# Optimization experiments

Measured on AMD Instinct MI355X. Metric: run time of the kernel, lower is better.

Reference implementation:

```python
import jax, jax.numpy as jnp
import numpy as np

B, N, IN_CH = 16, 2048, 128
H, C = 4, 64
HC = H * C
E = 524288
NT = B * N
FC0, FC1 = 1024, 512
OMIC = 128
OUT = 2
LN_EPS = 1e-5


def setup_inputs() -> dict:
    key = jax.random.key(0)
    ks = jax.random.split(key, 32)
    s = 0.02
    d = {}
    d['x'] = jax.random.normal(ks[0], (NT, IN_CH), jnp.float32)
    d['edge_index'] = jax.random.randint(ks[1], (2, E), 0, NT, dtype=jnp.int64)
    # GATConv 1: Linear(IN_CH, H*C, bias=False), att_src/att_dst [H,C], bias [H*C]
    d['w1'] = jax.random.normal(ks[2], (IN_CH, HC), jnp.float32) * s
    d['att_src1'] = jax.random.normal(ks[3], (H, C), jnp.float32) * s
    d['att_dst1'] = jax.random.normal(ks[4], (H, C), jnp.float32) * s
    d['bias1'] = jnp.zeros((HC,), jnp.float32)
    d['pool1_w'] = jax.random.normal(ks[5], (HC, 1), jnp.float32) * s
    d['pool1_b'] = jnp.zeros((1,), jnp.float32)
    # GATConv 2: in = H*C
    d['w2'] = jax.random.normal(ks[6], (HC, HC), jnp.float32) * s
    d['att_src2'] = jax.random.normal(ks[7], (H, C), jnp.float32) * s
    d['att_dst2'] = jax.random.normal(ks[8], (H, C), jnp.float32) * s
    d['bias2'] = jnp.zeros((HC,), jnp.float32)
    d['pool2_w'] = jax.random.normal(ks[9], (HC, 1), jnp.float32) * s
    d['pool2_b'] = jnp.zeros((1,), jnp.float32)
    # LayerNorm(num_nodes)
    d['ln_w'] = jnp.ones((N,), jnp.float32)
    d['ln_b'] = jnp.zeros((N,), jnp.float32)
    # FC encoder: Linear(3N, FC0)+ELU, Linear(FC0, FC1)+ELU, Linear(FC1, OMIC)+ELU
    d['enc0_w'] = jax.random.normal(ks[10], (3 * N, FC0), jnp.float32) * s
    d['enc0_b'] = jnp.zeros((FC0,), jnp.float32)
    d['enc1_w'] = jax.random.normal(ks[11], (FC0, FC1), jnp.float32) * s
    d['enc1_b'] = jnp.zeros((FC1,), jnp.float32)
    d['enc2_w'] = jax.random.normal(ks[12], (FC1, OMIC), jnp.float32) * s
    d['enc2_b'] = jnp.zeros((OMIC,), jnp.float32)
    d['last_w'] = jax.random.normal(ks[13], (OMIC, OUT), jnp.float32) * s
    d['last_b'] = jnp.zeros((OUT,), jnp.float32)
    return d


def layer_norm(v, w, b):
    mu = jnp.mean(v, axis=-1, keepdims=True)
    var = jnp.mean((v - mu) ** 2, axis=-1, keepdims=True)
    return (v - mu) * jax.lax.rsqrt(var + LN_EPS) * w + b


def gat_conv(x, src, dst, w, att_src, att_dst, bias):
    # x: [NT, F_in] -> transformed per head [NT, H, C]
    xw = (x @ w).reshape(NT, H, C)
    a_src = jnp.einsum('nhc,hc->nh', xw, att_src)  # [NT, H]
    a_dst = jnp.einsum('nhc,hc->nh', xw, att_dst)
    alpha = jax.nn.leaky_relu(a_src[src] + a_dst[dst], negative_slope=0.2)  # [E', H]
    amax = jax.ops.segment_max(alpha, dst, num_segments=NT)
    ea = jnp.exp(alpha - amax[dst])
    denom = jax.ops.segment_sum(ea, dst, num_segments=NT)
    coef = ea / (denom[dst] + 1e-16)
    msg = xw[src] * coef[:, :, None]  # [E', H, C]
    out = jax.ops.segment_sum(msg, dst, num_segments=NT)
    return out.reshape(NT, HC) + bias


def reference(x, edge_index, w1, att_src1, att_dst1, bias1, pool1_w, pool1_b,
              w2, att_src2, att_dst2, bias2, pool2_w, pool2_b,
              ln_w, ln_b, enc0_w, enc0_b, enc1_w, enc1_b, enc2_w, enc2_b,
              last_w, last_b):
    # add self-loops (GATConv default)
    loops = jnp.arange(NT, dtype=edge_index.dtype)
    src = jnp.concatenate([edge_index[0], loops])
    dst = jnp.concatenate([edge_index[1], loops])
    # layer1 feature: per-node mean, densified to [B, N]
    x0 = layer_norm(jnp.mean(x, axis=-1).reshape(B, N), ln_w, ln_b)
    # GAT layer 1 (dropout is identity in eval)
    h = jax.nn.elu(gat_conv(x, src, dst, w1, att_src1, att_dst1, bias1))
    x1 = layer_norm((h @ pool1_w + pool1_b)[:, 0].reshape(B, N), ln_w, ln_b)
    # GAT layer 2
    h = jax.nn.elu(gat_conv(h, src, dst, w2, att_src2, att_dst2, bias2))
    x2 = layer_norm((h @ pool2_w + pool2_b)[:, 0].reshape(B, N), ln_w, ln_b)
    feat = jnp.concatenate([x0, x1, x2], axis=1)  # [B, 3N]
    e = jax.nn.elu(feat @ enc0_w + enc0_b)
    e = jax.nn.elu(e @ enc1_w + enc1_b)
    e = jax.nn.elu(e @ enc2_w + enc2_b)
    return e @ last_w + last_b  # [B, OUT]
```

## Files before the change

### kernel.cpp

```cpp
#include <hip/hip_runtime.h>
#include <math.h>

#define NTN 32768
#define BB 16
#define NN 2048
#define IN_CH 128
#define HC 256
#define EREAL 524288
#define ETOT (EREAL + NTN)
#define FC0 1024
#define FC1 512
#define OMIC 128
#define OUTD 2
#define CAP 96

#define PREP_BLKS (NTN / 4)
#define DEG_BLKS (EREAL / 256)
#define CASTW_BLKS ((HC * IN_CH + HC * HC) / 256)
#define GEMM_YB (NTN / 128)
#define FILL_YB 512

typedef __attribute__((ext_vector_type(8))) short bf16x8;
typedef __attribute__((ext_vector_type(4))) float f32x4;
typedef __attribute__((ext_vector_type(2))) float f32x2;

static __device__ __forceinline__ float wave_sum(float v) {
    for (int o = 32; o; o >>= 1) v += __shfl_xor(v, o);
    return v;
}
static __device__ __forceinline__ unsigned short f2bf(float f) {
    unsigned u = __float_as_uint(f);
    unsigned r = (u + 0x7fff + ((u >> 16) & 1)) >> 16;
    return (unsigned short)r;
}
static __device__ __forceinline__ void pkfma(f32x2& acc, f32x2 ab, f32x2 e2) {
    asm("v_pk_fma_f32 %0, %1, %2, %0" : "+v"(acc) : "v"(ab), "v"(e2));
}
static __device__ __forceinline__ void fma8pk(uint4 v, f32x2 e2, f32x2* acc) {
    f32x2 p;
    p.x = __uint_as_float(v.x << 16); p.y = __uint_as_float(v.x & 0xffff0000u);
    pkfma(acc[0], p, e2);
    p.x = __uint_as_float(v.y << 16); p.y = __uint_as_float(v.y & 0xffff0000u);
    pkfma(acc[1], p, e2);
    p.x = __uint_as_float(v.z << 16); p.y = __uint_as_float(v.z & 0xffff0000u);
    pkfma(acc[2], p, e2);
    p.x = __uint_as_float(v.w << 16); p.y = __uint_as_float(v.w & 0xffff0000u);
    pkfma(acc[3], p, e2);
}
static __device__ __forceinline__ void dot2bf(float& acc, unsigned px, unsigned pe) {
    asm("v_dot2_f32_bf16 %0, %1, %2, %0" : "+v"(acc) : "v"(px), "v"(pe));
}
static __device__ __forceinline__ void dot8x2(uint4 a, uint4 b, unsigned pe, float* acc) {
    unsigned p;
    p = __builtin_amdgcn_perm(a.x, b.x, 0x01000504u); dot2bf(acc[0], p, pe);
    p = __builtin_amdgcn_perm(a.x, b.x, 0x03020706u); dot2bf(acc[1], p, pe);
    p = __builtin_amdgcn_perm(a.y, b.y, 0x01000504u); dot2bf(acc[2], p, pe);
    p = __builtin_amdgcn_perm(a.y, b.y, 0x03020706u); dot2bf(acc[3], p, pe);
    p = __builtin_amdgcn_perm(a.z, b.z, 0x01000504u); dot2bf(acc[4], p, pe);
    p = __builtin_amdgcn_perm(a.z, b.z, 0x03020706u); dot2bf(acc[5], p, pe);
    p = __builtin_amdgcn_perm(a.w, b.w, 0x01000504u); dot2bf(acc[6], p, pe);
    p = __builtin_amdgcn_perm(a.w, b.w, 0x03020706u); dot2bf(acc[7], p, pe);
}

__global__ __launch_bounds__(256) void k_pre(
    const float* __restrict__ x, unsigned short* __restrict__ xb, float* __restrict__ xmean,
    const int* __restrict__ ei, int* __restrict__ deg, int* __restrict__ epos,
    const float* __restrict__ w1, const float* __restrict__ w2,
    unsigned short* __restrict__ w1t, unsigned short* __restrict__ w2t) {
    int b = blockIdx.x, t = threadIdx.x;
    if (b < PREP_BLKS) {
        int wave = t >> 6, lane = t & 63;
        int n = b * 4 + wave;
        float2 v = *(const float2*)(x + (size_t)n * IN_CH + lane * 2);
        ushort2 o;
        o.x = f2bf(v.x); o.y = f2bf(v.y);
        *(ushort2*)(xb + (size_t)n * IN_CH + lane * 2) = o;
        float s = wave_sum(v.x + v.y);
        if (lane == 0) xmean[n] = s * (1.0f / 128.0f);
    } else if (b < PREP_BLKS + DEG_BLKS) {
        int e = (b - PREP_BLKS) * 256 + t;
        int d = ei[EREAL + e];
        epos[e] = atomicAdd(&deg[d], 1);
    } else {
        int idx = (b - PREP_BLKS - DEG_BLKS) * 256 + t;
        if (idx < HC * IN_CH) {
            int n = idx / IN_CH, k = idx % IN_CH;
            w1t[idx] = f2bf(w1[(size_t)k * HC + n]);
        } else {
            int j = idx - HC * IN_CH;
            int n = j / HC, k = j % HC;
            w2t[j] = f2bf(w2[(size_t)k * HC + n]);
        }
    }
}

__global__ __launch_bounds__(1024) void k_scan(const int* __restrict__ deg, int* __restrict__ rowptr,
                                               int* __restrict__ csr) {
    __shared__ int sd[1024];
    int t = threadIdx.x;
    int base = t * 32;
    int loc[32];
    int s = 0;
#pragma unroll
    for (int j = 0; j < 32; j++) { int d = deg[base + j] + 1; loc[j] = d; s += d; }
    sd[t] = s; __syncthreads();
    for (int o = 1; o < 1024; o <<= 1) {
        int v = (t >= o) ? sd[t - o] : 0;
        __syncthreads();
        sd[t] += v;
        __syncthreads();
    }
    int run = sd[t] - s;
#pragma unroll
    for (int j = 0; j < 32; j++) {
        rowptr[base + j] = run;
        csr[run] = base + j;
        run += loc[j];
    }
    if (t == 1023) rowptr[NTN] = run;
}

__global__ __launch_bounds__(256) void k_gemm_mfma(
    const unsigned short* __restrict__ A, const unsigned short* __restrict__ Bt, int K,
    const float* __restrict__ attS, const float* __restrict__ attD,
    unsigned short* __restrict__ Cout, float* __restrict__ aS, float* __restrict__ aD,
    const int* __restrict__ ei, const int* __restrict__ epos,
    const int* __restrict__ rowptr, int* __restrict__ csr) {
    __shared__ unsigned short As[128][72];
    __shared__ unsigned short Bs[64][72];
    const int t = threadIdx.x;
    const int bx = blockIdx.x, by = blockIdx.y;
    if (by >= GEMM_YB) {
        int e = (((by - GEMM_YB) * 4 + bx)) * 256 + t;
        int s = ei[e], d = ei[EREAL + e];
        csr[rowptr[d] + 1 + epos[e]] = s;
        return;
    }
    const int lane = t & 63, wave = t >> 6;
    const int quad = lane >> 4, l16 = lane & 15;
    const int arow = t >> 1, acol = (t & 1) * 32;
    const int brow = t >> 2, bcol = (t & 3) * 16;
    const unsigned short* Ag = A + (size_t)(by * 128 + arow) * K + acol;
    const unsigned short* Bg = Bt + (size_t)(bx * 64 + brow) * K + bcol;
    f32x4 acc[2][4] = {};
    for (int k0 = 0; k0 < K; k0 += 64) {
        uint4 a0 = *(const uint4*)(Ag + k0);
        uint4 a1 = *(const uint4*)(Ag + k0 + 8);
        uint4 a2 = *(const uint4*)(Ag + k0 + 16);
        uint4 a3 = *(const uint4*)(Ag + k0 + 24);
        uint4 b0 = *(const uint4*)(Bg + k0);
        uint4 b1 = *(const uint4*)(Bg + k0 + 8);
        __syncthreads();
        *(uint4*)&As[arow][acol +  0] = a0;
        *(uint4*)&As[arow][acol +  8] = a1;
        *(uint4*)&As[arow][acol + 16] = a2;
        *(uint4*)&As[arow][acol + 24] = a3;
        *(uint4*)&Bs[brow][bcol +  0] = b0;
        *(uint4*)&Bs[brow][bcol +  8] = b1;
        __syncthreads();
#pragma unroll
        for (int kc = 0; kc < 64; kc += 32) {
            bf16x8 af[2], bfr[4];
#pragma unroll
            for (int mt = 0; mt < 2; mt++)
                af[mt] = *(const bf16x8*)&As[wave * 32 + mt * 16 + l16][kc + quad * 8];
#pragma unroll
            for (int nt = 0; nt < 4; nt++)
                bfr[nt] = *(const bf16x8*)&Bs[nt * 16 + l16][kc + quad * 8];
#pragma unroll
            for (int mt = 0; mt < 2; mt++)
#pragma unroll
                for (int nt = 0; nt < 4; nt++)
                    acc[mt][nt] = __builtin_amdgcn_mfma_f32_16x16x32_bf16(af[mt], bfr[nt], acc[mt][nt], 0, 0, 0);
        }
    }
    float as_l[4], ad_l[4];
#pragma unroll
    for (int nt = 0; nt < 4; nt++) {
        int gcol = bx * 64 + nt * 16 + l16;
        as_l[nt] = attS[gcol];
        ad_l[nt] = attD[gcol];
    }
#pragma unroll
    for (int mt = 0; mt < 2; mt++) {
#pragma unroll
        for (int reg = 0; reg < 4; reg++) {
            int grow = by * 128 + wave * 32 + mt * 16 + quad * 4 + reg;
            float ps = 0.f, pd = 0.f;
#pragma unroll
            for (int nt = 0; nt < 4; nt++) {
                float v = acc[mt][nt][reg];
                Cout[(size_t)grow * HC + bx * 64 + nt * 16 + l16] = f2bf(v);
                ps += v * as_l[nt];
                pd += v * ad_l[nt];
            }
            for (int o = 8; o; o >>= 1) { ps += __shfl_xor(ps, o); pd += __shfl_xor(pd, o); }
            if (l16 == 0) { aS[grow * 4 + bx] = ps; aD[grow * 4 + bx] = pd; }
        }
    }
}

__global__ __launch_bounds__(256) void k_agg(
    const unsigned short* __restrict__ xw, const float* __restrict__ aS, const float* __restrict__ aD,
    const int* __restrict__ rowptr, const int* __restrict__ csr,
    const float* __restrict__ bias, const float* __restrict__ poolw, const float* __restrict__ poolb,
    unsigned short* __restrict__ hout, float* __restrict__ xpre) {
    __shared__ float ea_s[2][CAP][4];
    __shared__ float part[2][2][256];
    __shared__ float lpart[2][2][4];
    int t = threadIdx.x;
    int wave = t >> 6, lane = t & 63;
    int nd = wave >> 1, half = wave & 1;
    int n = blockIdx.x * 2 + nd;
    int beg = rowptr[n], end = rowptr[n + 1];
    int deg = end - beg;
    int mid = beg + ((deg + 1) >> 1);
    int wbeg = half ? mid : beg;
    int wend = half ? end : mid;
    float4 ad4 = *(const float4*)(aD + n * 4);
    if (deg <= CAP) {
        for (int i = wbeg + lane; i < wend; i += 64) {
            int s = csr[i];
            float4 as4 = *(const float4*)(aS + s * 4);
            float a0 = as4.x + ad4.x; a0 = a0 > 0.f ? a0 : 0.2f * a0;
            float a1 = as4.y + ad4.y; a1 = a1 > 0.f ? a1 : 0.2f * a1;
            float a2 = as4.z + ad4.z; a2 = a2 > 0.f ? a2 : 0.2f * a2;
            float a3 = as4.w + ad4.w; a3 = a3 > 0.f ? a3 : 0.2f * a3;
            float4 e4;
            e4.x = __expf(a0); e4.y = __expf(a1); e4.z = __expf(a2); e4.w = __expf(a3);
            *(float4*)&ea_s[nd][i - beg][0] = e4;
        }
    } else {
        float l0 = 0.f, l1 = 0.f, l2 = 0.f, l3 = 0.f;
        for (int i = wbeg + lane; i < wend; i += 64) {
            int s = csr[i];
            float4 as4 = *(const float4*)(aS + s * 4);
            float a0 = as4.x + ad4.x; a0 = a0 > 0.f ? a0 : 0.2f * a0; l0 += __expf(a0);
            float a1 = as4.y + ad4.y; a1 = a1 > 0.f ? a1 : 0.2f * a1; l1 += __expf(a1);
            float a2 = as4.z + ad4.z; a2 = a2 > 0.f ? a2 : 0.2f * a2; l2 += __expf(a2);
            float a3 = as4.w + ad4.w; a3 = a3 > 0.f ? a3 : 0.2f * a3; l3 += __expf(a3);
        }
        l0 = wave_sum(l0); l1 = wave_sum(l1); l2 = wave_sum(l2); l3 = wave_sum(l3);
        if (lane == 0) {
            lpart[nd][half][0] = l0; lpart[nd][half][1] = l1;
            lpart[nd][half][2] = l2; lpart[nd][half][3] = l3;
        }
    }
    __syncthreads();
    int l31 = lane & 31, hi = lane >> 5;
    int head = l31 >> 3;
    float acc8[8] = {};
    f32x2 accF[4] = {};
    unsigned t8 = (unsigned)(l31 * 8);
    if (deg <= CAP) {
        int i = wbeg;
        for (; i + 4 <= wend; i += 4) {
            int iA = i + 2 * hi;
            int sA = csr[iA], sB = csr[iA + 1];
            float eA = ea_s[nd][iA - beg][head];
            float eB = ea_s[nd][iA + 1 - beg][head];
            unsigned pe;
            asm("v_cvt_pk_bf16_f32 %0, %1, %2" : "=v"(pe) : "v"(eA), "v"(eB));
            uint4 vA = *(const uint4*)(xw + ((unsigned)sA * HC + t8));
            uint4 vB = *(const uint4*)(xw + ((unsigned)sB * HC + t8));
            dot8x2(vA, vB, pe, acc8);
        }
        if (i < wend) {
            int iA = i + 2 * hi, iB = iA + 1;
            bool okA = iA < wend, okB = iB < wend;
            int ia = iA - beg; if (ia > CAP - 1) ia = CAP - 1;
            int ib = iB - beg; if (ib > CAP - 1) ib = CAP - 1;
            int sA = csr[okA ? iA : wbeg];
            int sB = csr[okB ? iB : wbeg];
            float eA = okA ? ea_s[nd][ia][head] : 0.f;
            float eB = okB ? ea_s[nd][ib][head] : 0.f;
            unsigned pe;
            asm("v_cvt_pk_bf16_f32 %0, %1, %2" : "=v"(pe) : "v"(eA), "v"(eB));
            uint4 vA = *(const uint4*)(xw + ((unsigned)sA * HC + t8));
            uint4 vB = *(const uint4*)(xw + ((unsigned)sB * HC + t8));
            dot8x2(vA, vB, pe, acc8);
        }
    } else {
        const unsigned short* xwc = xw + t8;
        float adh = head == 0 ? ad4.x : head == 1 ? ad4.y : head == 2 ? ad4.z : ad4.w;
        for (int i = wbeg; i < wend; i += 2) {
            int idx = i + hi;
            bool ok = idx < wend;
            int sA = csr[ok ? idx : wbeg];
            float a = aS[sA * 4 + head] + adh;
            a = a > 0.f ? a : 0.2f * a;
            float eA = ok ? __expf(a) : 0.f;
            uint4 vA = *(const uint4*)(xwc + (size_t)sA * HC);
            f32x2 eA2; eA2.x = eA; eA2.y = eA;
            fma8pk(vA, eA2, accF);
        }
    }
    float r8[8];
#pragma unroll
    for (int j = 0; j < 8; j++) {
        float v = acc8[j] + accF[j >> 1][j & 1];
        v += __shfl_xor(v, 32);
        r8[j] = v;
    }
    if (hi == 0) {
        float4 q0; q0.x = r8[0]; q0.y = r8[1]; q0.z = r8[2]; q0.w = r8[3];
        float4 q1; q1.x = r8[4]; q1.y = r8[5]; q1.z = r8[6]; q1.w = r8[7];
        *(float4*)&part[nd][half][l31 * 8] = q0;
        *(float4*)&part[nd][half][l31 * 8 + 4] = q1;
    }
    __syncthreads();
    if (half == 0 && hi == 0) {
        float ilh;
        if (deg <= CAP) {
            float lsum = 0.f;
            for (int j = (l31 & 7); j < deg; j += 8) lsum += ea_s[nd][j][head];
            lsum += __shfl_xor(lsum, 1);
            lsum += __shfl_xor(lsum, 2);
            lsum += __shfl_xor(lsum, 4);
            ilh = 1.0f / (lsum + 1e-16f);
        } else {
            ilh = 1.0f / (lpart[nd][0][head] + lpart[nd][1][head] + 1e-16f);
        }
        float4 p00 = *(const float4*)&part[nd][0][l31 * 8];
        float4 p01 = *(const float4*)&part[nd][0][l31 * 8 + 4];
        float4 p10 = *(const float4*)&part[nd][1][l31 * 8];
        float4 p11 = *(const float4*)&part[nd][1][l31 * 8 + 4];
        float4 b0 = *(const float4*)(bias + l31 * 8);
        float4 b1 = *(const float4*)(bias + l31 * 8 + 4);
        float r[8];
        r[0] = (p00.x + p10.x) * ilh + b0.x;
        r[1] = (p00.y + p10.y) * ilh + b0.y;
        r[2] = (p00.z + p10.z) * ilh + b0.z;
        r[3] = (p00.w + p10.w) * ilh + b0.w;
        r[4] = (p01.x + p11.x) * ilh + b1.x;
        r[5] = (p01.y + p11.y) * ilh + b1.y;
        r[6] = (p01.z + p11.z) * ilh + b1.z;
        r[7] = (p01.w + p11.w) * ilh + b1.w;
#pragma unroll
        for (int j = 0; j < 8; j++) r[j] = r[j] > 0.f ? r[j] : expm1f(r[j]);
        if (hout) {
            uint4 o;
            o.x = (unsigned)f2bf(r[0]) | ((unsigned)f2bf(r[1]) << 16);
            o.y = (unsigned)f2bf(r[2]) | ((unsigned)f2bf(r[3]) << 16);
            o.z = (unsigned)f2bf(r[4]) | ((unsigned)f2bf(r[5]) << 16);
            o.w = (unsigned)f2bf(r[6]) | ((unsigned)f2bf(r[7]) << 16);
            *(uint4*)(hout + (size_t)n * HC + l31 * 8) = o;
        }
        float4 w0 = *(const float4*)(poolw + l31 * 8);
        float4 w1v = *(const float4*)(poolw + l31 * 8 + 4);
        float p = r[0] * w0.x + r[1] * w0.y + r[2] * w0.z + r[3] * w0.w +
                  r[4] * w1v.x + r[5] * w1v.y + r[6] * w1v.z + r[7] * w1v.w;
        for (int o = 16; o; o >>= 1) p += __shfl_xor(p, o);
        if (l31 == 0) xpre[n] = p + poolb[0];
    }
}

__global__ __launch_bounds__(256) void k_ln3(const float* __restrict__ xmean, const float* __restrict__ x1pre,
                                             const float* __restrict__ x2pre, const float* __restrict__ lw,
                                             const float* __restrict__ lb, float* __restrict__ feat) {
    __shared__ float r0[256], r1[256];
    int b = blockIdx.x, t = threadIdx.x;
    int row = b & 15, seg = b >> 4;
    const float* src = (seg == 0 ? xmean : seg == 1 ? x1pre : x2pre) + (size_t)row * NN;
    float* dst = feat + (size_t)row * (3 * NN) + seg * NN;
    float v[8];
    float s = 0.f, s2 = 0.f;
#pragma unroll
    for (int j = 0; j < 8; j++) {
        float x = src[t + j * 256];
        v[j] = x; s += x; s2 += x * x;
    }
    r0[t] = s; r1[t] = s2; __syncthreads();
    for (int o = 128; o; o >>= 1) {
        if (t < o) { r0[t] += r0[t + o]; r1[t] += r1[t + o]; }
        __syncthreads();
    }
    float mu = r0[0] * (1.0f / NN);
    float var = r1[0] * (1.0f / NN) - mu * mu;
    float rs = rsqrtf(var + 1e-5f);
#pragma unroll
    for (int j = 0; j < 8; j++) {
        int idx = t + j * 256;
        dst[idx] = (v[j] - mu) * rs * lw[idx] + lb[idx];
    }
}

template<int KC>
__global__ __launch_bounds__(256) void k_fc_splitk(const float* __restrict__ In, const float* __restrict__ W,
                                                   float* __restrict__ partial, int K, int Nc) {
    __shared__ float in_s[16][KC];
    int t = threadIdx.x;
    int k0 = blockIdx.y * KC;
    for (int idx = t; idx < 16 * KC; idx += 256) {
        int r = idx / KC, kk = idx % KC;
        in_s[r][kk] = In[(size_t)r * K + k0 + kk];
    }
    __syncthreads();
    int col = blockIdx.x * 256 + t;
    if (col < Nc) {
        float acc[16] = {};
#pragma unroll
        for (int kk = 0; kk < KC; kk++) {
            float w = W[(size_t)(k0 + kk) * Nc + col];
#pragma unroll
            for (int r = 0; r < 16; r++) acc[r] += in_s[r][kk] * w;
        }
        float* pp = partial + ((size_t)blockIdx.y * 16) * Nc + col;
#pragma unroll
        for (int r = 0; r < 16; r++) pp[(size_t)r * Nc] = acc[r];
    }
}

template<int KS>
__global__ __launch_bounds__(256) void k_fc_reduce(const float* __restrict__ partial, const float* __restrict__ bias,
                                                   float* __restrict__ Out, int Nc) {
    __shared__ float sm[256];
    int t = threadIdx.x;
    int col = blockIdx.x * 32 + (t & 31);
    int r = blockIdx.y;
    int h = t >> 5;
    float s = 0.f;
#pragma unroll
    for (int i = 0; i < KS / 8; i++)
        s += partial[((size_t)(h + 8 * i) * 16 + r) * Nc + col];
    sm[t] = s;
    __syncthreads();
    if (t < 32) {
        float v = sm[t] + sm[t + 32] + sm[t + 64] + sm[t + 96] +
                  sm[t + 128] + sm[t + 160] + sm[t + 192] + sm[t + 224];
        v += bias[col];
        v = v > 0.f ? v : expm1f(v);
        Out[(size_t)r * Nc + col] = v;
    }
}

__global__ __launch_bounds__(256) void k_last(const float* __restrict__ In, const float* __restrict__ W,
                                              const float* __restrict__ b, float* __restrict__ Out) {
    int t = threadIdx.x;
    int r = t >> 4, c = (t >> 3) & 1, ksub = t & 7;
    float s = 0.f;
#pragma unroll
    for (int k = 0; k < OMIC / 8; k++) s += In[r * OMIC + k * 8 + ksub] * W[(k * 8 + ksub) * OUTD + c];
    for (int o = 1; o < 8; o <<= 1) s += __shfl_xor(s, o);
    if (ksub == 0) Out[r * OUTD + c] = s + b[c];
}

extern "C" void kernel_launch(void* const* d_in, const int* in_sizes, int n_in,
                              void* d_out, int out_size, void* d_ws, size_t ws_size,
                              hipStream_t stream) {
    (void)in_sizes; (void)n_in; (void)out_size; (void)ws_size;
    const float* x        = (const float*)d_in[0];
    const int*   ei       = (const int*)d_in[1];
    const float* w1       = (const float*)d_in[2];
    const float* att_src1 = (const float*)d_in[3];
    const float* att_dst1 = (const float*)d_in[4];
    const float* bias1    = (const float*)d_in[5];
    const float* pool1_w  = (const float*)d_in[6];
    const float* pool1_b  = (const float*)d_in[7];
    const float* w2       = (const float*)d_in[8];
    const float* att_src2 = (const float*)d_in[9];
    const float* att_dst2 = (const float*)d_in[10];
    const float* bias2    = (const float*)d_in[11];
    const float* pool2_w  = (const float*)d_in[12];
    const float* pool2_b  = (const float*)d_in[13];
    const float* ln_w     = (const float*)d_in[14];
    const float* ln_b     = (const float*)d_in[15];
    const float* enc0_w   = (const float*)d_in[16];
    const float* enc0_b   = (const float*)d_in[17];
    const float* enc1_w   = (const float*)d_in[18];
    const float* enc1_b   = (const float*)d_in[19];
    const float* enc2_w   = (const float*)d_in[20];
    const float* enc2_b   = (const float*)d_in[21];
    const float* last_w   = (const float*)d_in[22];
    const float* last_b   = (const float*)d_in[23];
    float* out = (float*)d_out;

    char* p = (char*)d_ws;
    auto alloc = [&](size_t bytes) -> void* {
        void* r = (void*)p;
        p += (bytes + 255) & ~(size_t)255;
        return r;
    };
    unsigned short* xwb  = (unsigned short*)alloc((size_t)NTN * HC * 2);
    unsigned short* hb   = (unsigned short*)alloc((size_t)NTN * HC * 2);
    unsigned short* xb   = (unsigned short*)alloc((size_t)NTN * IN_CH * 2);
    unsigned short* w1t  = (unsigned short*)alloc((size_t)HC * IN_CH * 2);
    unsigned short* w2t  = (unsigned short*)alloc((size_t)HC * HC * 2);
    float* a_src  = (float*)alloc((size_t)NTN * 4 * 4);
    float* a_dst  = (float*)alloc((size_t)NTN * 4 * 4);
    float* xmean  = (float*)alloc((size_t)NTN * 4);
    float* x1pre  = (float*)alloc((size_t)NTN * 4);
    float* x2pre  = (float*)alloc((size_t)NTN * 4);
    float* feat   = (float*)alloc((size_t)BB * 3 * NN * 4);
    float* e0     = (float*)alloc((size_t)BB * FC0 * 4);
    float* e1     = (float*)alloc((size_t)BB * FC1 * 4);
    float* e2     = (float*)alloc((size_t)BB * OMIC * 4);
    float* part0  = (float*)alloc((size_t)96 * 16 * FC0 * 4);
    float* part1  = (float*)alloc((size_t)64 * 16 * FC1 * 4);
    float* part2  = (float*)alloc((size_t)32 * 16 * OMIC * 4);
    int*   deg    = (int*)alloc((size_t)NTN * 4);
    int*   rowptr = (int*)alloc((size_t)(NTN + 1) * 4);
    int*   epos   = (int*)alloc((size_t)EREAL * 4);
    int*   csr    = (int*)alloc((size_t)ETOT * 4);

    hipMemsetAsync(deg, 0, (size_t)NTN * 4, stream);

    k_pre<<<PREP_BLKS + DEG_BLKS + CASTW_BLKS, 256, 0, stream>>>(
        x, xb, xmean, ei, deg, epos, w1, w2, w1t, w2t);
    k_scan<<<1, 1024, 0, stream>>>(deg, rowptr, csr);

    k_gemm_mfma<<<dim3(4, GEMM_YB + FILL_YB), 256, 0, stream>>>(
        xb, w1t, IN_CH, att_src1, att_dst1, xwb, a_src, a_dst, ei, epos, rowptr, csr);
    k_agg<<<NTN / 2, 256, 0, stream>>>(xwb, a_src, a_dst, rowptr, csr, bias1, pool1_w, pool1_b, hb, x1pre);

    k_gemm_mfma<<<dim3(4, GEMM_YB), 256, 0, stream>>>(
        hb, w2t, HC, att_src2, att_dst2, xwb, a_src, a_dst, ei, epos, rowptr, csr);
    k_agg<<<NTN / 2, 256, 0, stream>>>(xwb, a_src, a_dst, rowptr, csr, bias2, pool2_w, pool2_b, (unsigned short*)nullptr, x2pre);

    k_ln3<<<48, 256, 0, stream>>>(xmean, x1pre, x2pre, ln_w, ln_b, feat);

    k_fc_splitk<64><<<dim3(4, 96), 256, 0, stream>>>(feat, enc0_w, part0, 3 * NN, FC0);
    k_fc_reduce<96><<<dim3(FC0 / 32, 16), 256, 0, stream>>>(part0, enc0_b, e0, FC0);
    k_fc_splitk<16><<<dim3(2, 64), 256, 0, stream>>>(e0, enc1_w, part1, FC0, FC1);
    k_fc_reduce<64><<<dim3(FC1 / 32, 16), 256, 0, stream>>>(part1, enc1_b, e1, FC1);
    k_fc_splitk<16><<<dim3(1, 32), 256, 0, stream>>>(e1, enc2_w, part2, FC1, OMIC);
    k_fc_reduce<32><<<dim3(OMIC / 32, 16), 256, 0, stream>>>(part2, enc2_b, e2, OMIC);
    k_last<<<1, 256, 0, stream>>>(e2, last_w, last_b, out);
}
```

Before: 340.6 us.

## Assign one wave per node in GAT aggregation and deepen gather unrolling

The aggregation kernel now handles four nodes per block, one wavefront per node, instead of splitting each node's edges across two waves. This removes the cross-wave LDS partial-sum exchange and both block-wide barriers. Source byte offsets are cached in LDS so the gather loop no longer rereads csr, and the main loop is unrolled to gather 16 neighbor rows per iteration to keep more loads in flight. In exchange, each node's edge loop runs serially within a single wave, and the extra unrolling raises register pressure.

Result: faster. 315.7 us (-7.3%).

```diff
diff --git a/kernel.cpp b/kernel.cpp
--- a/kernel.cpp
+++ b/kernel.cpp
@@ -32,6 +32,10 @@
     unsigned u = __float_as_uint(f);
     unsigned r = (u + 0x7fff + ((u >> 16) & 1)) >> 16;
     return (unsigned short)r;
+}
+static __device__ __forceinline__ void wave_sync() {
+    asm volatile("s_waitcnt lgkmcnt(0)" ::: "memory");
+    __builtin_amdgcn_sched_barrier(0);
 }
 static __device__ __forceinline__ void pkfma(f32x2& acc, f32x2 ab, f32x2 e2) {
     asm("v_pk_fma_f32 %0, %1, %2, %0" : "+v"(acc) : "v"(ab), "v"(e2));
@@ -205,22 +209,19 @@
     const int* __restrict__ rowptr, const int* __restrict__ csr,
     const float* __restrict__ bias, const float* __restrict__ poolw, const float* __restrict__ poolb,
     unsigned short* __restrict__ hout, float* __restrict__ xpre) {
-    __shared__ float ea_s[2][CAP][4];
-    __shared__ float part[2][2][256];
-    __shared__ float lpart[2][2][4];
+    __shared__ float ea_s[4][CAP][4];
+    __shared__ int   ss[4][CAP];
     int t = threadIdx.x;
-    int wave = t >> 6, lane = t & 63;
-    int nd = wave >> 1, half = wave & 1;
-    int n = blockIdx.x * 2 + nd;
+    int w = t >> 6, lane = t & 63;
+    int n = blockIdx.x * 4 + w;
     int beg = rowptr[n], end = rowptr[n + 1];
     int deg = end - beg;
-    int mid = beg + ((deg + 1) >> 1);
-    int wbeg = half ? mid : beg;
-    int wend = half ? end : mid;
     float4 ad4 = *(const float4*)(aD + n * 4);
+    float l0 = 0.f, l1 = 0.f, l2 = 0.f, l3 = 0.f;
     if (deg <= CAP) {
-        for (int i = wbeg + lane; i < wend; i += 64) {
-            int s = csr[i];
+        for (int i = lane; i < deg; i += 64) {
+            int s = csr[beg + i];
+            ss[w][i] = s << 9;
             float4 as4 = *(const float4*)(aS + s * 4);
             float a0 = as4.x + ad4.x; a0 = a0 > 0.f ? a0 : 0.2f * a0;
             float a1 = as4.y + ad4.y; a1 = a1 > 0.f ? a1 : 0.2f * a1;
@@ -228,12 +229,12 @@
             float a3 = as4.w + ad4.w; a3 = a3 > 0.f ? a3 : 0.2f * a3;
             float4 e4;
             e4.x = __expf(a0); e4.y = __expf(a1); e4.z = __expf(a2); e4.w = __expf(a3);
-            *(float4*)&ea_s[nd][i - beg][0] = e4;
-        }
+            *(float4*)&ea_s[w][i][0] = e4;
+        }
+        wave_sync();
     } else {
-        float l0 = 0.f, l1 = 0.f, l2 = 0.f, l3 = 0.f;
-        for (int i = wbeg + lane; i < wend; i += 64) {
-            int s = csr[i];
+        for (int i = lane; i < deg; i += 64) {
+            int s = csr[beg + i];
             float4 as4 = *(const float4*)(aS + s * 4);
             float a0 = as4.x + ad4.x; a0 = a0 > 0.f ? a0 : 0.2f * a0; l0 += __expf(a0);
             float a1 = as4.y + ad4.y; a1 = a1 > 0.f ? a1 : 0.2f * a1; l1 += __expf(a1);
@@ -241,52 +242,87 @@
             float a3 = as4.w + ad4.w; a3 = a3 > 0.f ? a3 : 0.2f * a3; l3 += __expf(a3);
         }
         l0 = wave_sum(l0); l1 = wave_sum(l1); l2 = wave_sum(l2); l3 = wave_sum(l3);
-        if (lane == 0) {
-            lpart[nd][half][0] = l0; lpart[nd][half][1] = l1;
-            lpart[nd][half][2] = l2; lpart[nd][half][3] = l3;
-        }
-    }
-    __syncthreads();
+    }
     int l31 = lane & 31, hi = lane >> 5;
     int head = l31 >> 3;
     float acc8[8] = {};
     f32x2 accF[4] = {};
-    unsigned t8 = (unsigned)(l31 * 8);
+    unsigned tb = (unsigned)(l31 * 16);
+    const char* xwb_ = (const char*)xw;
     if (deg <= CAP) {
-        int i = wbeg;
-        for (; i + 4 <= wend; i += 4) {
+        int i = 0;
+        for (; i + 16 <= deg; i += 16) {
+            int iA = i + 8 * hi;
+            int o0 = ss[w][iA], o1 = ss[w][iA + 1], o2 = ss[w][iA + 2], o3 = ss[w][iA + 3];
+            int o4 = ss[w][iA + 4], o5 = ss[w][iA + 5], o6 = ss[w][iA + 6], o7 = ss[w][iA + 7];
+            float e0 = ea_s[w][iA][head],     e1 = ea_s[w][iA + 1][head];
+            float e2 = ea_s[w][iA + 2][head], e3 = ea_s[w][iA + 3][head];
+            float e4 = ea_s[w][iA + 4][head], e5 = ea_s[w][iA + 5][head];
+            float e6 = ea_s[w][iA + 6][head], e7 = ea_s[w][iA + 7][head];
+            uint4 v0 = *(const uint4*)(xwb_ + ((unsigned)o0 + tb));
+            uint4 v1 = *(const uint4*)(xwb_ + ((unsigned)o1 + tb));
+            uint4 v2 = *(const uint4*)(xwb_ + ((unsigned)o2 + tb));
+            uint4 v3 = *(const uint4*)(xwb_ + ((unsigned)o3 + tb));
+            uint4 v4 = *(const uint4*)(xwb_ + ((unsigned)o4 + tb));
+            uint4 v5 = *(const uint4*)(xwb_ + ((unsigned)o5 + tb));
+            uint4 v6 = *(const uint4*)(xwb_ + ((unsigned)o6 + tb));
+            uint4 v7 = *(const uint4*)(xwb_ + ((unsigned)o7 + tb));
+            unsigned p01, p23, p45, p67;
+            asm("v_cvt_pk_bf16_f32 %0, %1, %2" : "=v"(p01) : "v"(e0), "v"(e1));
+            asm("v_cvt_pk_bf16_f32 %0, %1, %2" : "=v"(p23) : "v"(e2), "v"(e3));
+            asm("v_cvt_pk_bf16_f32 %0, %1, %2" : "=v"(p45) : "v"(e4), "v"(e5));
+            asm("v_cvt_pk_bf16_f32 %0, %1, %2" : "=v"(p67) : "v"(e6), "v"(e7));
+            dot8x2(v0, v1, p01, acc8);
+            dot8x2(v2, v3, p23, acc8);
+            dot8x2(v4, v5, p45, acc8);
+            dot8x2(v6, v7, p67, acc8);
+        }
+        for (; i + 8 <= deg; i += 8) {
+            int iA = i + 4 * hi;
+            int o0 = ss[w][iA], o1 = ss[w][iA + 1], o2 = ss[w][iA + 2], o3 = ss[w][iA + 3];
+            float e0 = ea_s[w][iA][head],     e1 = ea_s[w][iA + 1][head];
+            float e2 = ea_s[w][iA + 2][head], e3 = ea_s[w][iA + 3][head];
+            uint4 v0 = *(const uint4*)(xwb_ + ((unsigned)o0 + tb));
+            uint4 v1 = *(const uint4*)(xwb_ + ((unsigned)o1 + tb));
+            uint4 v2 = *(const uint4*)(xwb_ + ((unsigned)o2 + tb));
+            uint4 v3 = *(const uint4*)(xwb_ + ((unsigned)o3 + tb));
+            unsigned p01, p23;
+            asm("v_cvt_pk_bf16_f32 %0, %1, %2" : "=v"(p01) : "v"(e0), "v"(e1));
+            asm("v_cvt_pk_bf16_f32 %0, %1, %2" : "=v"(p23) : "v"(e2), "v"(e3));
+            dot8x2(v0, v1, p01, acc8);
+            dot8x2(v2, v3, p23, acc8);
+        }
+        for (; i + 4 <= deg; i += 4) {
             int iA = i + 2 * hi;
-            int sA = csr[iA], sB = csr[iA + 1];
-            float eA = ea_s[nd][iA - beg][head];
-            float eB = ea_s[nd][iA + 1 - beg][head];
+            int o0 = ss[w][iA], o1 = ss[w][iA + 1];
+            float e0 = ea_s[w][iA][head], e1 = ea_s[w][iA + 1][head];
             unsigned pe;
-            asm("v_cvt_pk_bf16_f32 %0, %1, %2" : "=v"(pe) : "v"(eA), "v"(eB));
-            uint4 vA = *(const uint4*)(xw + ((unsigned)sA * HC + t8));
-            uint4 vB = *(const uint4*)(xw + ((unsigned)sB * HC + t8));
-            dot8x2(vA, vB, pe, acc8);
-        }
-        if (i < wend) {
+            asm("v_cvt_pk_bf16_f32 %0, %1, %2" : "=v"(pe) : "v"(e0), "v"(e1));
+            uint4 v0 = *(const uint4*)(xwb_ + ((unsigned)o0 + tb));
+            uint4 v1 = *(const uint4*)(xwb_ + ((unsigned)o1 + tb));
+            dot8x2(v0, v1, pe, acc8);
+        }
+        if (i < deg) {
             int iA = i + 2 * hi, iB = iA + 1;
-            bool okA = iA < wend, okB = iB < wend;
-            int ia = iA - beg; if (ia > CAP - 1) ia = CAP - 1;
-            int ib = iB - beg; if (ib > CAP - 1) ib = CAP - 1;
-            int sA = csr[okA ? iA : wbeg];
-            int sB = csr[okB ? iB : wbeg];
-            float eA = okA ? ea_s[nd][ia][head] : 0.f;
-            float eB = okB ? ea_s[nd][ib][head] : 0.f;
+            bool okA = iA < deg, okB = iB < deg;
+            int ia = okA ? iA : 0;
+            int ib = okB ? iB : 0;
+            int o0 = ss[w][ia], o1 = ss[w][ib];
+            float e0 = okA ? ea_s[w][ia][head] : 0.f;
+            float e1 = okB ? ea_s[w][ib][head] : 0.f;
             unsigned pe;
-            asm("v_cvt_pk_bf16_f32 %0, %1, %2" : "=v"(pe) : "v"(eA), "v"(eB));
-            uint4 vA = *(const uint4*)(xw + ((unsigned)sA * HC + t8));
-            uint4 vB = *(const uint4*)(xw + ((unsigned)sB * HC + t8));
-            dot8x2(vA, vB, pe, acc8);
+            asm("v_cvt_pk_bf16_f32 %0, %1, %2" : "=v"(pe) : "v"(e0), "v"(e1));
+            uint4 v0 = *(const uint4*)(xwb_ + ((unsigned)o0 + tb));
+            uint4 v1 = *(const uint4*)(xwb_ + ((unsigned)o1 + tb));
+            dot8x2(v0, v1, pe, acc8);
         }
     } else {
-        const unsigned short* xwc = xw + t8;
+        const unsigned short* xwc = xw + l31 * 8;
         float adh = head == 0 ? ad4.x : head == 1 ? ad4.y : head == 2 ? ad4.z : ad4.w;
-        for (int i = wbeg; i < wend; i += 2) {
+        for (int i = beg; i < end; i += 2) {
             int idx = i + hi;
-            bool ok = idx < wend;
-            int sA = csr[ok ? idx : wbeg];
+            bool ok = idx < end;
+            int sA = csr[ok ? idx : beg];
             float a = aS[sA * 4 + head] + adh;
             a = a > 0.f ? a : 0.2f * a;
             float eA = ok ? __expf(a) : 0.f;
@@ -303,39 +339,29 @@
         r8[j] = v;
     }
     if (hi == 0) {
-        float4 q0; q0.x = r8[0]; q0.y = r8[1]; q0.z = r8[2]; q0.w = r8[3];
-        float4 q1; q1.x = r8[4]; q1.y = r8[5]; q1.z = r8[6]; q1.w = r8[7];
-        *(float4*)&part[nd][half][l31 * 8] = q0;
-        *(float4*)&part[nd][half][l31 * 8 + 4] = q1;
-    }
-    __syncthreads();
-    if (half == 0 && hi == 0) {
         float ilh;
         if (deg <= CAP) {
             float lsum = 0.f;
-            for (int j = (l31 & 7); j < deg; j += 8) lsum += ea_s[nd][j][head];
+            for (int j = (l31 & 7); j < deg; j += 8) lsum += ea_s[w][j][head];
             lsum += __shfl_xor(lsum, 1);
             lsum += __shfl_xor(lsum, 2);
             lsum += __shfl_xor(lsum, 4);
             ilh = 1.0f / (lsum + 1e-16f);
         } else {
-            ilh = 1.0f / (lpart[nd][0][head] + lpart[nd][1][head] + 1e-16f);
-        }
-        float4 p00 = *(const float4*)&part[nd][0][l31 * 8];
-        float4 p01 = *(const float4*)&part[nd][0][l31 * 8 + 4];
-        float4 p10 = *(const float4*)&part[nd][1][l31 * 8];
-        float4 p11 = *(const float4*)&part[nd][1][l31 * 8 + 4];
+            float lh = head == 0 ? l0 : head == 1 ? l1 : head == 2 ? l2 : l3;
+            ilh = 1.0f / (lh + 1e-16f);
+        }
         float4 b0 = *(const float4*)(bias + l31 * 8);
         float4 b1 = *(const float4*)(bias + l31 * 8 + 4);
         float r[8];
-        r[0] = (p00.x + p10.x) * ilh + b0.x;
-        r[1] = (p00.y + p10.y) * ilh + b0.y;
-        r[2] = (p00.z + p10.z) * ilh + b0.z;
-        r[3] = (p00.w + p10.w) * ilh + b0.w;
-        r[4] = (p01.x + p11.x) * ilh + b1.x;
-        r[5] = (p01.y + p11.y) * ilh + b1.y;
-        r[6] = (p01.z + p11.z) * ilh + b1.z;
-        r[7] = (p01.w + p11.w) * ilh + b1.w;
+        r[0] = r8[0] * ilh + b0.x;
+        r[1] = r8[1] * ilh + b0.y;
+        r[2] = r8[2] * ilh + b0.z;
+        r[3] = r8[3] * ilh + b0.w;
+        r[4] = r8[4] * ilh + b1.x;
+        r[5] = r8[5] * ilh + b1.y;
+        r[6] = r8[6] * ilh + b1.z;
+        r[7] = r8[7] * ilh + b1.w;
 #pragma unroll
         for (int j = 0; j < 8; j++) r[j] = r[j] > 0.f ? r[j] : expm1f(r[j]);
         if (hout) {
@@ -511,11 +537,11 @@
 
     k_gemm_mfma<<<dim3(4, GEMM_YB + FILL_YB), 256, 0, stream>>>(
         xb, w1t, IN_CH, att_src1, att_dst1, xwb, a_src, a_dst, ei, epos, rowptr, csr);
-    k_agg<<<NTN / 2, 256, 0, stream>>>(xwb, a_src, a_dst, rowptr, csr, bias1, pool1_w, pool1_b, hb, x1pre);
+    k_agg<<<NTN / 4, 256, 0, stream>>>(xwb, a_src, a_dst, rowptr, csr, bias1, pool1_w, pool1_b, hb, x1pre);
 
     k_gemm_mfma<<<dim3(4, GEMM_YB), 256, 0, stream>>>(
         hb, w2t, HC, att_src2, att_dst2, xwb, a_src, a_dst, ei, epos, rowptr, csr);
-    k_agg<<<NTN / 2, 256, 0, stream>>>(xwb, a_src, a_dst, rowptr, csr, bias2, pool2_w, pool2_b, (unsigned short*)nullptr, x2pre);
+    k_agg<<<NTN / 4, 256, 0, stream>>>(xwb, a_src, a_dst, rowptr, csr, bias2, pool2_w, pool2_b, (unsigned short*)nullptr, x2pre);
 
     k_ln3<<<48, 256, 0, stream>>>(xmean, x1pre, x2pre, ln_w, ln_b, feat);
 
```
